# Performance work log

Measured on AMD Instinct MI355X. Metric: run time of the kernel, lower is better.

Reference implementation:

```python
import jax, jax.numpy as jnp
import numpy as np

B, S, E, H = 4, 2048, 1024, 16
D = E // H  # head_dim = 64


def setup_inputs() -> dict:
    key = jax.random.key(0)
    k1, k2, k3 = jax.random.split(key, 3)
    x = jax.random.normal(k1, (B, S, E), dtype=jnp.float32)
    w_attn = jax.random.normal(k2, (E, 3 * E), dtype=jnp.float32) * (E ** -0.5)
    b_attn = jnp.zeros((3 * E,), dtype=jnp.float32)
    w_out = jax.random.normal(k3, (E, E), dtype=jnp.float32) * (E ** -0.5)
    b_out = jnp.zeros((E,), dtype=jnp.float32)
    return {"x": x, "w_attn": w_attn, "b_attn": b_attn, "w_out": w_out, "b_out": b_out}


def reference(x, w_attn, b_attn, w_out, b_out):
    b, s, e = x.shape
    qkv = x @ w_attn + b_attn                      # [b, s, 3e]
    q, k, v = jnp.split(qkv, 3, axis=2)
    q = q.reshape(b, s, H, D)
    k = k.reshape(b, s, H, D)
    v = v.reshape(b, s, H, D)
    energy = jnp.einsum('nqhd,nkhd->nhqk', q, k)   # [b, H, s, s]
    causal = jnp.tril(jnp.ones((s, s), dtype=bool))
    energy = jnp.where(causal, energy, -jnp.inf)
    scale = jnp.sqrt(jnp.float32(D))
    attn = jax.nn.softmax(energy / scale, axis=-1)  # dropout_rate=0.0 -> identity
    out = jnp.einsum('nhql,nlhd->nqhd', attn, v).reshape(b, s, e)
    return out @ w_out + b_out
```

## Files before the change

### kernel.cpp

```cpp
#include <hip/hip_runtime.h>

typedef short bf16x8 __attribute__((ext_vector_type(8)));
typedef float f32x4 __attribute__((ext_vector_type(4)));
typedef float f32x16 __attribute__((ext_vector_type(16)));
typedef float float4v __attribute__((ext_vector_type(4)));
typedef short short4v __attribute__((ext_vector_type(4)));
typedef unsigned uint2v __attribute__((ext_vector_type(2)));
typedef unsigned uint4v __attribute__((ext_vector_type(4)));

#define B_ 4
#define S_ 2048
#define E_ 1024
#define H_ 16
#define D_ 64
#define M_ (B_*S_)
#define N1_ (3*E_)

__device__ inline short f2bs(float f) {
    unsigned u = __builtin_bit_cast(unsigned, f);
    unsigned r = u + 0x7fffu + ((u >> 16) & 1u);
    return (short)(r >> 16);
}
__device__ inline float exp2a(float x) {
    float r; asm("v_exp_f32 %0, %1" : "=v"(r) : "v"(x)); return r;
}
__device__ inline unsigned cvtpk(float a, float b) {
    unsigned r; asm("v_cvt_pk_bf16_f32 %0, %1, %2" : "=v"(r) : "v"(a), "v"(b)); return r;
}

__device__ inline const __attribute__((address_space(1))) void* gas(const void* p) {
    return (const __attribute__((address_space(1))) void*)p;
}
__device__ inline __attribute__((address_space(3))) void* las(void* p) {
    return (__attribute__((address_space(3))) void*)p;
}

__global__ void convert_f32_bf16(const float* __restrict__ in, short* __restrict__ out, int n) {
    int tid = blockIdx.x * blockDim.x + threadIdx.x;
    int stride = gridDim.x * blockDim.x;
    for (int i = tid * 4; i < n; i += stride * 4) {
        float4v v = *(const float4v*)&in[i];
        short4v o;
        o[0] = f2bs(v[0]); o[1] = f2bs(v[1]); o[2] = f2bs(v[2]); o[3] = f2bs(v[3]);
        *(short4v*)&out[i] = o;
    }
}

__global__ void transpose_convert(const float* __restrict__ in, short* __restrict__ out,
                                  int rows, int cols) {
    __shared__ float t[32][33];
    int bx = blockIdx.x * 32;
    int by = blockIdx.y * 32;
    int tx = threadIdx.x, ty = threadIdx.y;
#pragma unroll
    for (int i = 0; i < 4; ++i)
        t[ty + i * 8][tx] = in[(size_t)(by + ty + i * 8) * cols + bx + tx];
    __syncthreads();
#pragma unroll
    for (int i = 0; i < 4; ++i)
        out[(size_t)(bx + ty + i * 8) * rows + by + tx] = f2bs(t[tx][ty + i * 8]);
}

#define VMW(n) asm volatile("s_waitcnt vmcnt(" #n ")" ::: "memory")
#define NOP_ ((void)0)

#define QKV_MFMA(Q) \
    _Pragma("unroll") for (int nf = 0; nf < 6; ++nf) { \
        acc[(Q)][nf] = __builtin_amdgcn_mfma_f32_16x16x32_bf16(af[0], bfrag[nf][0], acc[(Q)][nf], 0, 0, 0); \
        acc[(Q)][nf] = __builtin_amdgcn_mfma_f32_16x16x32_bf16(af[1], bfrag[nf][1], acc[(Q)][nf], 0, 0, 0); \
    }

#define QKV_PHASE(Q, STAGE_STMT, WAITV) do { \
    bf16x8 af[2]; \
    const char* lAq = lA + (Q) * 4096; \
    _Pragma("unroll") for (int ks = 0; ks < 2; ++ks) \
        af[ks] = *(const bf16x8*)(lAq + li * 128 + ((ks * 64 + g * 16) ^ ((li & 7) << 4))); \
    STAGE_STMT; \
    __builtin_amdgcn_s_barrier(); \
    asm volatile("s_waitcnt lgkmcnt(0)" ::: "memory"); \
    __builtin_amdgcn_sched_barrier(0); \
    __builtin_amdgcn_s_setprio(1); \
    QKV_MFMA(Q); \
    __builtin_amdgcn_s_setprio(0); \
    WAITV; \
    __builtin_amdgcn_s_barrier(); \
} while (0)

__global__ __launch_bounds__(256, 2) void gemm_qkv(
    const short* __restrict__ A, const short* __restrict__ Bt,
    const float* __restrict__ bias,
    short* __restrict__ Qb, short* __restrict__ Kb, short* __restrict__ Vt) {
    __shared__ __attribute__((aligned(16))) short ldsA[2][8192];
    __shared__ __attribute__((aligned(16))) short ldsB[2][12288];
    const int tid = threadIdx.x;
    const int lane = tid & 63;
    const int wid = tid >> 6;
    const int li = lane & 15, g = lane >> 4;
    const int wr = wid >> 1, wc = wid & 1;
    const int Kdim = E_;
    const int NT = Kdim >> 6;

    const int id = blockIdx.x;
    const int swz = (id & 7) * 128 + (id >> 3);
    const int bx = swz & 15, by = swz >> 4;
    const int row0 = by * 128, col0 = bx * 192;

    const int lr8 = lane >> 3;
    const int cstage = (((lane & 7) ^ (lr8 & 7)) << 4);

    auto stageA = [&](int buf, int kt) {
#pragma unroll
        for (int Q = 0; Q < 4; ++Q) {
            int grow = (wid >> 1) * 64 + Q * 16 + (wid & 1) * 8 + lr8;
            const char* src = (const char*)A +
                ((size_t)(row0 + grow) * Kdim + kt * 64) * 2 + cstage;
            char* dst = (char*)&ldsA[buf][0] + Q * 4096 + wid * 1024;
            __builtin_amdgcn_global_load_lds(gas(src), las(dst), 16, 0, 0);
        }
    };
    auto stageB = [&](int buf, int kt) {
#pragma unroll
        for (int i = 0; i < 6; ++i) {
            int grow = i * 32 + wid * 8 + lr8;
            const char* src = (const char*)Bt +
                ((size_t)(col0 + grow) * Kdim + kt * 64) * 2 + cstage;
            char* dst = (char*)&ldsB[buf][0] + i * 4096 + wid * 1024;
            __builtin_amdgcn_global_load_lds(gas(src), las(dst), 16, 0, 0);
        }
    };

    f32x4 acc[4][6];
#pragma unroll
    for (int m = 0; m < 4; ++m)
#pragma unroll
        for (int n = 0; n < 6; ++n) acc[m][n] = (f32x4){0.f, 0.f, 0.f, 0.f};

    stageB(0, 0);
    stageA(0, 0);
    asm volatile("s_waitcnt vmcnt(0)" ::: "memory");
    __syncthreads();

    for (int t = 0; t < NT; ++t) {
        const int cur = t & 1;
        const int nb = cur ^ 1;
        const int tn = t + 1;
        const bool st = (tn < NT);
        const char* lA = (const char*)&ldsA[cur][0] + wr * 2048;
        const char* lB = (const char*)&ldsB[cur][0];

        bf16x8 bfrag[6][2];
#pragma unroll
        for (int nf = 0; nf < 6; ++nf)
#pragma unroll
            for (int ks = 0; ks < 2; ++ks) {
                int r = wc * 96 + nf * 16 + li;
                bfrag[nf][ks] = *(const bf16x8*)(lB + r * 128 + ((ks * 64 + g * 16) ^ ((r & 7) << 4)));
            }
        if (st) {
            QKV_PHASE(0, stageB(nb, tn), NOP_);
            QKV_PHASE(1, stageA(nb, tn), VMW(8));
            QKV_PHASE(2, NOP_, NOP_);
            QKV_PHASE(3, NOP_, VMW(2));
        } else {
            QKV_PHASE(0, NOP_, NOP_);
            QKV_PHASE(1, NOP_, VMW(0));
            QKV_PHASE(2, NOP_, NOP_);
            QKV_PHASE(3, NOP_, NOP_);
        }
    }

#pragma unroll
    for (int nf = 0; nf < 6; ++nf) {
        int ncolg = col0 + wc * 96 + nf * 16 + li;
        float bv = bias[ncolg];
        int part = ncolg >> 10;
        int rem = ncolg & 1023;
        if (part < 2) {
            short* Dst = (part == 0) ? Qb : Kb;
#pragma unroll
            for (int mi = 0; mi < 4; ++mi) {
                int rbase = row0 + wr * 64 + mi * 16 + 4 * g;
#pragma unroll
                for (int j = 0; j < 4; ++j)
                    Dst[(size_t)(rbase + j) * E_ + rem] = f2bs(acc[mi][nf][j] + bv);
            }
        } else {
            int h = rem >> 6, d = rem & 63;
#pragma unroll
            for (int mi = 0; mi < 4; ++mi) {
                int s0 = row0 + wr * 64 + mi * 16 + 4 * g;
                int bb2 = s0 >> 11;
                int ss = s0 & 2047;
                uint2v p;
                p[0] = cvtpk(acc[mi][nf][0] + bv, acc[mi][nf][1] + bv);
                p[1] = cvtpk(acc[mi][nf][2] + bv, acc[mi][nf][3] + bv);
                *(uint2v*)&Vt[((size_t)(bb2 * H_ + h) * D_ + d) * S_ + ss] = p;
            }
        }
    }
}

#define MFMA8(Q) \
    _Pragma("unroll") for (int mf = 0; mf < 2; ++mf) \
    _Pragma("unroll") for (int nf = 0; nf < 2; ++nf) { \
        acc[(Q)*2+mf][nf] = __builtin_amdgcn_mfma_f32_16x16x32_bf16(af[mf][0], bfrag[nf][0], acc[(Q)*2+mf][nf], 0, 0, 0); \
        acc[(Q)*2+mf][nf] = __builtin_amdgcn_mfma_f32_16x16x32_bf16(af[mf][1], bfrag[nf][1], acc[(Q)*2+mf][nf], 0, 0, 0); \
    }

#define PHASE8(Q, STAGE_STMT, WAITV) do { \
    bf16x8 af[2][2]; \
    _Pragma("unroll") for (int mf = 0; mf < 2; ++mf) \
    _Pragma("unroll") for (int ks = 0; ks < 2; ++ks) { \
        int r = (Q)*32 + mf*16 + li; \
        af[mf][ks] = *(const bf16x8*)(lA + r*128 + ((ks*64 + g*16) ^ ((r & 7) << 4))); \
    } \
    STAGE_STMT; \
    __builtin_amdgcn_s_barrier(); \
    asm volatile("s_waitcnt lgkmcnt(0)" ::: "memory"); \
    __builtin_amdgcn_sched_barrier(0); \
    __builtin_amdgcn_s_setprio(1); \
    MFMA8(Q); \
    __builtin_amdgcn_s_setprio(0); \
    WAITV; \
    __builtin_amdgcn_s_barrier(); \
} while (0)

__global__ __launch_bounds__(512, 2) void gemm_out8(
    const short* __restrict__ A, const short* __restrict__ Bt,
    const float* __restrict__ bias, float* __restrict__ Cf) {
    __shared__ __attribute__((aligned(16))) short ldsA[2][2][2][4096];
    __shared__ __attribute__((aligned(16))) short ldsB[2][8192];
    const int tid = threadIdx.x;
    const int lane = tid & 63;
    const int wid = tid >> 6;
    const int li = lane & 15, g = lane >> 4;
    const int wr = wid >> 2, wc = wid & 3;
    const int Kdim = E_;
    const int NT = Kdim >> 6;

    const int id = blockIdx.x;
    const int swz = (id & 7) * 32 + (id >> 3);
    const int bx = swz & 7, by = swz >> 3;
    const int row0 = by * 256, col0 = bx * 128;

    const int rstage = wid * 8 + (lane >> 3);
    const int cstage = (((lane & 7) ^ ((lane >> 3) & 7)) << 4);

    auto stageA = [&](int buf, int kt, int seg) {
#pragma unroll
        for (int h = 0; h < 2; ++h) {
            const char* src = (const char*)A +
                ((size_t)(row0 + h * 128 + seg * 64 + rstage) * Kdim + kt * 64) * 2 + cstage;
            char* dst = (char*)&ldsA[buf][h][seg][0] + wid * 1024;
            __builtin_amdgcn_global_load_lds(gas(src), las(dst), 16, 0, 0);
        }
    };
    auto stageB = [&](int buf, int kt) {
#pragma unroll
        for (int i = 0; i < 2; ++i) {
            const char* src = (const char*)Bt +
                ((size_t)(col0 + i * 64 + rstage) * Kdim + kt * 64) * 2 + cstage;
            char* dst = (char*)&ldsB[buf][0] + i * 8192 + wid * 1024;
            __builtin_amdgcn_global_load_lds(gas(src), las(dst), 16, 0, 0);
        }
    };

    f32x4 acc[8][2];
#pragma unroll
    for (int m = 0; m < 8; ++m)
#pragma unroll
        for (int n = 0; n < 2; ++n) acc[m][n] = (f32x4){0.f, 0.f, 0.f, 0.f};

    stageB(0, 0);
    stageA(0, 0, 0);
    stageA(0, 0, 1);
    asm volatile("s_waitcnt vmcnt(0)" ::: "memory");
    __syncthreads();

    for (int t = 0; t < NT; ++t) {
        const int cur = t & 1;
        const int nb = cur ^ 1;
        const int tn = t + 1;
        const bool st = (tn < NT);
        const char* lA = (const char*)&ldsA[cur][wr][0][0];
        const char* lB = (const char*)&ldsB[cur][0];

        bf16x8 bfrag[2][2];
#pragma unroll
        for (int nf = 0; nf < 2; ++nf)
#pragma unroll
            for (int ks = 0; ks < 2; ++ks) {
                int r = wc * 32 + nf * 16 + li;
                bfrag[nf][ks] = *(const bf16x8*)(lB + r * 128 + ((ks * 64 + g * 16) ^ ((r & 7) << 4)));
            }
        if (st) {
            PHASE8(0, stageB(nb, tn), NOP_);
            PHASE8(1, stageA(nb, tn, 0), VMW(4));
            PHASE8(2, stageA(nb, tn, 1), NOP_);
            PHASE8(3, NOP_, VMW(2));
        } else {
            PHASE8(0, NOP_, NOP_);
            PHASE8(1, NOP_, VMW(0));
            PHASE8(2, NOP_, NOP_);
            PHASE8(3, NOP_, NOP_);
        }
    }

#pragma unroll
    for (int nf = 0; nf < 2; ++nf) {
        int ncol = col0 + wc * 32 + nf * 16 + li;
        float bv = bias[ncol];
#pragma unroll
        for (int mi = 0; mi < 8; ++mi) {
            int rbase = row0 + wr * 128 + mi * 16 + 4 * g;
#pragma unroll
            for (int j = 0; j < 4; ++j)
                Cf[(size_t)(rbase + j) * E_ + ncol] = acc[mi][nf][j] + bv;
        }
    }
}

#define GRP 1040
__global__ __launch_bounds__(256, 4) void attn_kernel(
    const short* __restrict__ Qb, const short* __restrict__ Kb,
    const short* __restrict__ Vt, short* __restrict__ Ob) {
    __shared__ __attribute__((aligned(16))) char Kl[8 * GRP];
    __shared__ __attribute__((aligned(16))) char Vl[8 * GRP];
    const int lane = threadIdx.x & 63;
    const int wv = threadIdx.x >> 6;
    const int l31 = lane & 31;
    const int hi = lane >> 5;
    const int id = blockIdx.x;
    const int xcd = id & 7;
    const int r_ = id >> 3;
    const int qt = 15 - (r_ >> 3);
    const int bh = xcd * 8 + (r_ & 7);
    const int bb = bh >> 4, hh = bh & 15;
    const short* Qh = Qb + (size_t)bb * (S_ * E_) + hh * 64;
    const short* Kh = Kb + (size_t)bb * (S_ * E_) + hh * 64;
    const short* Vh = Vt + (size_t)bh * (D_ * S_);
    const float CEXP = 0.18033688011112042f;

    const int rstage = wv * 8 + (lane >> 3);
    const int cstage = (((lane & 7) ^ ((lane >> 3) & 7)) << 4);

    const int q0w = qt * 128 + wv * 32;
    const int q = q0w + l31;

    bf16x8 qf[4];
#pragma unroll
    for (int c = 0; c < 4; ++c)
        qf[c] = *(const bf16x8*)&Qh[(size_t)q * E_ + c * 16 + hi * 8];

    f32x16 acc[2];
#pragma unroll
    for (int d = 0; d < 2; ++d)
#pragma unroll
        for (int r = 0; r < 16; ++r) acc[d][r] = 0.f;
    float m = -3e38f, mC = 0.f, l = 0.f;

    const int nw = (q0w + 95) >> 6;
    const int nt = (qt * 128 + 191) >> 6;

    const int kg0 = (l31 >> 3) * GRP + (l31 & 7) * 128;
    const int kg1 = ((32 + l31) >> 3) * GRP + (l31 & 7) * 128;
    const int ksw = (l31 & 7) << 4;

    for (int it = 0; it < nt; ++it) {
        const int kt0 = it * 64;
#pragma unroll
        for (int half = 0; half < 2; ++half) {
            const int grp = half * 4 + wv;
            const char* gk = (const char*)(Kh + (size_t)(kt0 + half * 32 + rstage) * E_) + cstage;
            __builtin_amdgcn_global_load_lds(gas(gk), las(Kl + grp * GRP), 16, 0, 0);
            const char* gv = (const char*)Vh + (size_t)(half * 32 + rstage) * (S_ * 2) + (size_t)kt0 * 2 + cstage;
            __builtin_amdgcn_global_load_lds(gas(gv), las(Vl + grp * GRP), 16, 0, 0);
        }
        __syncthreads();
        if (it < nw) {
            f32x16 sc0, sc1;
#pragma unroll
            for (int r = 0; r < 16; ++r) { sc0[r] = 0.f; sc1[r] = 0.f; }
#pragma unroll
            for (int c = 0; c < 4; ++c) {
                bf16x8 kf0 = *(const bf16x8*)(Kl + kg0 + ((c * 32 + hi * 16) ^ ksw));
                bf16x8 kf1 = *(const bf16x8*)(Kl + kg1 + ((c * 32 + hi * 16) ^ ksw));
                sc0 = __builtin_amdgcn_mfma_f32_32x32x16_bf16(kf0, qf[c], sc0, 0, 0, 0);
                sc1 = __builtin_amdgcn_mfma_f32_32x32x16_bf16(kf1, qf[c], sc1, 0, 0, 0);
            }
            if (kt0 + 63 > q0w) {
                const int kb = kt0 + 4 * hi;
#pragma unroll
                for (int r = 0; r < 16; ++r) {
                    int key = kb + (r & 3) + 8 * (r >> 2);
                    sc0[r] = (key > q) ? -3e38f : sc0[r];
                    sc1[r] = (key + 32 > q) ? -3e38f : sc1[r];
                }
            }
            float tmx[8];
#pragma unroll
            for (int r = 0; r < 8; ++r)
                tmx[r] = fmaxf(fmaxf(sc0[2 * r], sc0[2 * r + 1]),
                               fmaxf(sc1[2 * r], sc1[2 * r + 1]));
            float tm = fmaxf(fmaxf(fmaxf(tmx[0], tmx[1]), fmaxf(tmx[2], tmx[3])),
                             fmaxf(fmaxf(tmx[4], tmx[5]), fmaxf(tmx[6], tmx[7])));
            tm = fmaxf(tm, __shfl_xor(tm, 32, 64));
            bool need = (tm > m + 16.0f);
            if (__ballot((int)need) != 0ull) {
                float mn = fmaxf(m, tm);
                float sf = exp2a((m - mn) * CEXP);
                m = mn; mC = mn * CEXP;
                l *= sf;
#pragma unroll
                for (int d = 0; d < 2; ++d)
#pragma unroll
                    for (int r = 0; r < 16; ++r) acc[d][r] *= sf;
            }
#pragma unroll
            for (int r = 0; r < 16; ++r) {
                sc0[r] = exp2a(fmaf(sc0[r], CEXP, -mC));
                sc1[r] = exp2a(fmaf(sc1[r], CEXP, -mC));
            }
            float s0 = 0.f, s1 = 0.f;
#pragma unroll
            for (int r = 0; r < 8; ++r) {
                s0 += sc0[2 * r] + sc0[2 * r + 1];
                s1 += sc1[2 * r] + sc1[2 * r + 1];
            }
            float ls = s0 + s1;
            ls += __shfl_xor(ls, 32, 64);
            l += ls;
            bf16x8 pf[4];
#pragma unroll
            for (int s = 0; s < 2; ++s) {
                const f32x16& p = s ? sc1 : sc0;
                unsigned a0 = cvtpk(p[0], p[1]),   a1 = cvtpk(p[2], p[3]);
                unsigned b0 = cvtpk(p[4], p[5]),   b1 = cvtpk(p[6], p[7]);
                unsigned a2 = cvtpk(p[8], p[9]),   a3 = cvtpk(p[10], p[11]);
                unsigned b2 = cvtpk(p[12], p[13]), b3 = cvtpk(p[14], p[15]);
                asm volatile("v_permlane32_swap_b32 %0, %1" : "+v"(a0), "+v"(b0));
                asm volatile("v_permlane32_swap_b32 %0, %1" : "+v"(a1), "+v"(b1));
                asm volatile("v_permlane32_swap_b32 %0, %1" : "+v"(a2), "+v"(b2));
                asm volatile("v_permlane32_swap_b32 %0, %1" : "+v"(a3), "+v"(b3));
                uint4v u1, u2;
                u1[0] = a0; u1[1] = a1; u1[2] = b0; u1[3] = b1;
                u2[0] = a2; u2[1] = a3; u2[2] = b2; u2[3] = b3;
                pf[s * 2] = __builtin_bit_cast(bf16x8, u1);
                pf[s * 2 + 1] = __builtin_bit_cast(bf16x8, u2);
            }
#pragma unroll
            for (int db = 0; db < 2; ++db) {
                const int row = db * 32 + l31;
                const int rsw = (row & 7) << 4;
                const char* vrow = Vl + (row >> 3) * GRP + (row & 7) * 128;
                bf16x8 v0 = *(const bf16x8*)(vrow + ((hi * 16) ^ rsw));
                bf16x8 v1 = *(const bf16x8*)(vrow + ((32 + hi * 16) ^ rsw));
                bf16x8 v2 = *(const bf16x8*)(vrow + ((64 + hi * 16) ^ rsw));
                bf16x8 v3 = *(const bf16x8*)(vrow + ((96 + hi * 16) ^ rsw));
                acc[db] = __builtin_amdgcn_mfma_f32_32x32x16_bf16(v0, pf[0], acc[db], 0, 0, 0);
                acc[db] = __builtin_amdgcn_mfma_f32_32x32x16_bf16(v1, pf[1], acc[db], 0, 0, 0);
                acc[db] = __builtin_amdgcn_mfma_f32_32x32x16_bf16(v2, pf[2], acc[db], 0, 0, 0);
                acc[db] = __builtin_amdgcn_mfma_f32_32x32x16_bf16(v3, pf[3], acc[db], 0, 0, 0);
            }
        }
        __syncthreads();
    }

    float rl = __builtin_amdgcn_rcpf(l);
    short* orow = Ob + ((size_t)(bb * S_ + q)) * E_ + hh * 64;
#pragma unroll
    for (int db = 0; db < 2; ++db)
#pragma unroll
        for (int rb = 0; rb < 4; ++rb) {
            uint2v pk;
            pk[0] = cvtpk(acc[db][rb * 4 + 0] * rl, acc[db][rb * 4 + 1] * rl);
            pk[1] = cvtpk(acc[db][rb * 4 + 2] * rl, acc[db][rb * 4 + 3] * rl);
            *(uint2v*)&orow[db * 32 + rb * 8 + hi * 4] = pk;
        }
}

extern "C" void kernel_launch(void* const* d_in, const int* in_sizes, int n_in,
                              void* d_out, int out_size, void* d_ws, size_t ws_size,
                              hipStream_t stream) {
    const float* x      = (const float*)d_in[0];
    const float* w_attn = (const float*)d_in[1];
    const float* b_attn = (const float*)d_in[2];
    const float* w_out  = (const float*)d_in[3];
    const float* b_out  = (const float*)d_in[4];
    float* out = (float*)d_out;

    char* ws = (char*)d_ws;
    short* Xbf  = (short*)(ws);
    short* Wat  = (short*)(ws + (16ull << 20));
    short* Wot  = (short*)(ws + (22ull << 20));
    short* Qb   = (short*)(ws + (24ull << 20));
    short* Kb   = (short*)(ws + (40ull << 20));
    short* Vt   = (short*)(ws + (56ull << 20));
    short* Obuf = Xbf;

    convert_f32_bf16<<<2048, 256, 0, stream>>>(x, Xbf, M_ * E_);
    transpose_convert<<<dim3(N1_ / 32, E_ / 32), dim3(32, 8), 0, stream>>>(w_attn, Wat, E_, N1_);
    transpose_convert<<<dim3(E_ / 32, E_ / 32), dim3(32, 8), 0, stream>>>(w_out, Wot, E_, E_);

    gemm_qkv<<<1024, 256, 0, stream>>>(Xbf, Wat, b_attn, Qb, Kb, Vt);

    attn_kernel<<<1024, 256, 0, stream>>>(Qb, Kb, Vt, Obuf);

    gemm_out8<<<256, 512, 0, stream>>>(Obuf, Wot, b_out, out);
}
```

Measured before the change: 162.6 us.

## Merge prologue conversions into one launch and retile output GEMM to 128x128

The three preprocessing kernels (activation bf16 convert and two weight transpose-converts) become a single kernel that dispatches on block index, removing two launches and their gaps. The output projection GEMM moves from 512-thread blocks with 256x128 tiles to 256-thread blocks with 128x128 tiles and a 2x2 wave layout, doubling the grid to 512 blocks. Each wave now computes 64x64 with more B fragments held in registers. The trade-offs are less A reuse per block and more register pressure per wave, in return for better CU coverage.

New measurement: 155.5 us. 1.05x faster.

```diff
diff --git a/kernel.cpp b/kernel.cpp
--- a/kernel.cpp
+++ b/kernel.cpp
@@ -35,30 +35,44 @@
     return (__attribute__((address_space(3))) void*)p;
 }
 
-__global__ void convert_f32_bf16(const float* __restrict__ in, short* __restrict__ out, int n) {
-    int tid = blockIdx.x * blockDim.x + threadIdx.x;
-    int stride = gridDim.x * blockDim.x;
-    for (int i = tid * 4; i < n; i += stride * 4) {
-        float4v v = *(const float4v*)&in[i];
-        short4v o;
-        o[0] = f2bs(v[0]); o[1] = f2bs(v[1]); o[2] = f2bs(v[2]); o[3] = f2bs(v[3]);
-        *(short4v*)&out[i] = o;
-    }
-}
-
-__global__ void transpose_convert(const float* __restrict__ in, short* __restrict__ out,
-                                  int rows, int cols) {
+__global__ __launch_bounds__(256) void prologue(
+    const float* __restrict__ x, short* __restrict__ Xbf,
+    const float* __restrict__ w_attn, short* __restrict__ Wat,
+    const float* __restrict__ w_out, short* __restrict__ Wot) {
     __shared__ float t[32][33];
-    int bx = blockIdx.x * 32;
-    int by = blockIdx.y * 32;
-    int tx = threadIdx.x, ty = threadIdx.y;
-#pragma unroll
-    for (int i = 0; i < 4; ++i)
-        t[ty + i * 8][tx] = in[(size_t)(by + ty + i * 8) * cols + bx + tx];
-    __syncthreads();
-#pragma unroll
-    for (int i = 0; i < 4; ++i)
-        out[(size_t)(bx + ty + i * 8) * rows + by + tx] = f2bs(t[tx][ty + i * 8]);
+    const int bid = blockIdx.x;
+    const int tid = threadIdx.x;
+    if (bid < 2048) {
+        const int n = M_ * E_;
+        const int stride = 2048 * 256 * 4;
+        for (int i = (bid * 256 + tid) * 4; i < n; i += stride) {
+            float4v v = *(const float4v*)&x[i];
+            short4v o;
+            o[0] = f2bs(v[0]); o[1] = f2bs(v[1]); o[2] = f2bs(v[2]); o[3] = f2bs(v[3]);
+            *(short4v*)&Xbf[i] = o;
+        }
+    } else {
+        const float* in;
+        short* out;
+        int rows, cols, bx, by;
+        if (bid < 5120) {
+            in = w_attn; out = Wat; rows = E_; cols = N1_;
+            int b2 = bid - 2048;
+            bx = (b2 % 96) * 32; by = (b2 / 96) * 32;
+        } else {
+            in = w_out; out = Wot; rows = E_; cols = E_;
+            int b2 = bid - 5120;
+            bx = (b2 & 31) * 32; by = (b2 >> 5) * 32;
+        }
+        const int tx = tid & 31, ty = tid >> 5;
+#pragma unroll
+        for (int i = 0; i < 4; ++i)
+            t[ty + i * 8][tx] = in[(size_t)(by + ty + i * 8) * cols + bx + tx];
+        __syncthreads();
+#pragma unroll
+        for (int i = 0; i < 4; ++i)
+            out[(size_t)(bx + ty + i * 8) * rows + by + tx] = f2bs(t[tx][ty + i * 8]);
+    }
 }
 
 #define VMW(n) asm volatile("s_waitcnt vmcnt(" #n ")" ::: "memory")
@@ -200,80 +214,78 @@
     }
 }
 
-#define MFMA8(Q) \
-    _Pragma("unroll") for (int mf = 0; mf < 2; ++mf) \
-    _Pragma("unroll") for (int nf = 0; nf < 2; ++nf) { \
-        acc[(Q)*2+mf][nf] = __builtin_amdgcn_mfma_f32_16x16x32_bf16(af[mf][0], bfrag[nf][0], acc[(Q)*2+mf][nf], 0, 0, 0); \
-        acc[(Q)*2+mf][nf] = __builtin_amdgcn_mfma_f32_16x16x32_bf16(af[mf][1], bfrag[nf][1], acc[(Q)*2+mf][nf], 0, 0, 0); \
-    }
-
-#define PHASE8(Q, STAGE_STMT, WAITV) do { \
-    bf16x8 af[2][2]; \
-    _Pragma("unroll") for (int mf = 0; mf < 2; ++mf) \
-    _Pragma("unroll") for (int ks = 0; ks < 2; ++ks) { \
-        int r = (Q)*32 + mf*16 + li; \
-        af[mf][ks] = *(const bf16x8*)(lA + r*128 + ((ks*64 + g*16) ^ ((r & 7) << 4))); \
-    } \
+#define OUT_MFMA(Q) \
+    _Pragma("unroll") for (int nf = 0; nf < 4; ++nf) { \
+        acc[(Q)][nf] = __builtin_amdgcn_mfma_f32_16x16x32_bf16(af[0], bfrag[nf][0], acc[(Q)][nf], 0, 0, 0); \
+        acc[(Q)][nf] = __builtin_amdgcn_mfma_f32_16x16x32_bf16(af[1], bfrag[nf][1], acc[(Q)][nf], 0, 0, 0); \
+    }
+
+#define OUT_PHASE(Q, STAGE_STMT, WAITV) do { \
+    bf16x8 af[2]; \
+    const char* lAq = lA + (Q) * 4096; \
+    _Pragma("unroll") for (int ks = 0; ks < 2; ++ks) \
+        af[ks] = *(const bf16x8*)(lAq + li * 128 + ((ks * 64 + g * 16) ^ ((li & 7) << 4))); \
     STAGE_STMT; \
     __builtin_amdgcn_s_barrier(); \
     asm volatile("s_waitcnt lgkmcnt(0)" ::: "memory"); \
     __builtin_amdgcn_sched_barrier(0); \
     __builtin_amdgcn_s_setprio(1); \
-    MFMA8(Q); \
+    OUT_MFMA(Q); \
     __builtin_amdgcn_s_setprio(0); \
     WAITV; \
     __builtin_amdgcn_s_barrier(); \
 } while (0)
 
-__global__ __launch_bounds__(512, 2) void gemm_out8(
+__global__ __launch_bounds__(256, 2) void gemm_out(
     const short* __restrict__ A, const short* __restrict__ Bt,
     const float* __restrict__ bias, float* __restrict__ Cf) {
-    __shared__ __attribute__((aligned(16))) short ldsA[2][2][2][4096];
+    __shared__ __attribute__((aligned(16))) short ldsA[2][8192];
     __shared__ __attribute__((aligned(16))) short ldsB[2][8192];
     const int tid = threadIdx.x;
     const int lane = tid & 63;
     const int wid = tid >> 6;
     const int li = lane & 15, g = lane >> 4;
-    const int wr = wid >> 2, wc = wid & 3;
+    const int wr = wid >> 1, wc = wid & 1;
     const int Kdim = E_;
     const int NT = Kdim >> 6;
 
     const int id = blockIdx.x;
-    const int swz = (id & 7) * 32 + (id >> 3);
+    const int swz = (id & 7) * 64 + (id >> 3);
     const int bx = swz & 7, by = swz >> 3;
-    const int row0 = by * 256, col0 = bx * 128;
-
-    const int rstage = wid * 8 + (lane >> 3);
-    const int cstage = (((lane & 7) ^ ((lane >> 3) & 7)) << 4);
-
-    auto stageA = [&](int buf, int kt, int seg) {
-#pragma unroll
-        for (int h = 0; h < 2; ++h) {
+    const int row0 = by * 128, col0 = bx * 128;
+
+    const int lr8 = lane >> 3;
+    const int cstage = (((lane & 7) ^ (lr8 & 7)) << 4);
+
+    auto stageA = [&](int buf, int kt) {
+#pragma unroll
+        for (int Q = 0; Q < 4; ++Q) {
+            int grow = (wid >> 1) * 64 + Q * 16 + (wid & 1) * 8 + lr8;
             const char* src = (const char*)A +
-                ((size_t)(row0 + h * 128 + seg * 64 + rstage) * Kdim + kt * 64) * 2 + cstage;
-            char* dst = (char*)&ldsA[buf][h][seg][0] + wid * 1024;
+                ((size_t)(row0 + grow) * Kdim + kt * 64) * 2 + cstage;
+            char* dst = (char*)&ldsA[buf][0] + Q * 4096 + wid * 1024;
             __builtin_amdgcn_global_load_lds(gas(src), las(dst), 16, 0, 0);
         }
     };
     auto stageB = [&](int buf, int kt) {
 #pragma unroll
-        for (int i = 0; i < 2; ++i) {
+        for (int i = 0; i < 4; ++i) {
+            int grow = i * 32 + wid * 8 + lr8;
             const char* src = (const char*)Bt +
-                ((size_t)(col0 + i * 64 + rstage) * Kdim + kt * 64) * 2 + cstage;
-            char* dst = (char*)&ldsB[buf][0] + i * 8192 + wid * 1024;
+                ((size_t)(col0 + grow) * Kdim + kt * 64) * 2 + cstage;
+            char* dst = (char*)&ldsB[buf][0] + i * 4096 + wid * 1024;
             __builtin_amdgcn_global_load_lds(gas(src), las(dst), 16, 0, 0);
         }
     };
 
-    f32x4 acc[8][2];
-#pragma unroll
-    for (int m = 0; m < 8; ++m)
-#pragma unroll
-        for (int n = 0; n < 2; ++n) acc[m][n] = (f32x4){0.f, 0.f, 0.f, 0.f};
+    f32x4 acc[4][4];
+#pragma unroll
+    for (int m = 0; m < 4; ++m)
+#pragma unroll
+        for (int n = 0; n < 4; ++n) acc[m][n] = (f32x4){0.f, 0.f, 0.f, 0.f};
 
     stageB(0, 0);
-    stageA(0, 0, 0);
-    stageA(0, 0, 1);
+    stageA(0, 0);
     asm volatile("s_waitcnt vmcnt(0)" ::: "memory");
     __syncthreads();
 
@@ -282,37 +294,37 @@
         const int nb = cur ^ 1;
         const int tn = t + 1;
         const bool st = (tn < NT);
-        const char* lA = (const char*)&ldsA[cur][wr][0][0];
+        const char* lA = (const char*)&ldsA[cur][0] + wr * 2048;
         const char* lB = (const char*)&ldsB[cur][0];
 
-        bf16x8 bfrag[2][2];
-#pragma unroll
-        for (int nf = 0; nf < 2; ++nf)
+        bf16x8 bfrag[4][2];
+#pragma unroll
+        for (int nf = 0; nf < 4; ++nf)
 #pragma unroll
             for (int ks = 0; ks < 2; ++ks) {
-                int r = wc * 32 + nf * 16 + li;
+                int r = wc * 64 + nf * 16 + li;
                 bfrag[nf][ks] = *(const bf16x8*)(lB + r * 128 + ((ks * 64 + g * 16) ^ ((r & 7) << 4)));
             }
         if (st) {
-            PHASE8(0, stageB(nb, tn), NOP_);
-            PHASE8(1, stageA(nb, tn, 0), VMW(4));
-            PHASE8(2, stageA(nb, tn, 1), NOP_);
-            PHASE8(3, NOP_, VMW(2));
+            OUT_PHASE(0, stageB(nb, tn), NOP_);
+            OUT_PHASE(1, stageA(nb, tn), VMW(8));
+            OUT_PHASE(2, NOP_, NOP_);
+            OUT_PHASE(3, NOP_, VMW(2));
         } else {
-            PHASE8(0, NOP_, NOP_);
-            PHASE8(1, NOP_, VMW(0));
-            PHASE8(2, NOP_, NOP_);
-            PHASE8(3, NOP_, NOP_);
-        }
-    }
-
-#pragma unroll
-    for (int nf = 0; nf < 2; ++nf) {
-        int ncol = col0 + wc * 32 + nf * 16 + li;
+            OUT_PHASE(0, NOP_, NOP_);
+            OUT_PHASE(1, NOP_, VMW(0));
+            OUT_PHASE(2, NOP_, NOP_);
+            OUT_PHASE(3, NOP_, NOP_);
+        }
+    }
+
+#pragma unroll
+    for (int nf = 0; nf < 4; ++nf) {
+        int ncol = col0 + wc * 64 + nf * 16 + li;
         float bv = bias[ncol];
 #pragma unroll
-        for (int mi = 0; mi < 8; ++mi) {
-            int rbase = row0 + wr * 128 + mi * 16 + 4 * g;
+        for (int mi = 0; mi < 4; ++mi) {
+            int rbase = row0 + wr * 64 + mi * 16 + 4 * g;
 #pragma unroll
             for (int j = 0; j < 4; ++j)
                 Cf[(size_t)(rbase + j) * E_ + ncol] = acc[mi][nf][j] + bv;
@@ -498,13 +510,11 @@
     short* Vt   = (short*)(ws + (56ull << 20));
     short* Obuf = Xbf;
 
-    convert_f32_bf16<<<2048, 256, 0, stream>>>(x, Xbf, M_ * E_);
-    transpose_convert<<<dim3(N1_ / 32, E_ / 32), dim3(32, 8), 0, stream>>>(w_attn, Wat, E_, N1_);
-    transpose_convert<<<dim3(E_ / 32, E_ / 32), dim3(32, 8), 0, stream>>>(w_out, Wot, E_, E_);
+    prologue<<<6144, 256, 0, stream>>>(x, Xbf, w_attn, Wat, w_out, Wot);
 
     gemm_qkv<<<1024, 256, 0, stream>>>(Xbf, Wat, b_attn, Qb, Kb, Vt);
 
     attn_kernel<<<1024, 256, 0, stream>>>(Qb, Kb, Vt, Obuf);
 
-    gemm_out8<<<256, 512, 0, stream>>>(Obuf, Wot, b_out, out);
-}
+    gemm_out<<<512, 256, 0, stream>>>(Obuf, Wot, b_out, out);
+}
```
